# Kernel tuning notes

Hardware: AMD Instinct MI355X
Metric: run time of the kernel (lower is better)

Reference implementation:

```python
import jax, jax.numpy as jnp
import numpy as np

B, N, D, DEPTH = 1, 512, 128, 4


def mlp_apply(W, x):
    # W: (depth, d, d), x: (..., d). First layer has no activation, then silu before each matmul.
    x = x @ W[0]
    for i in range(1, DEPTH):
        x = jax.nn.silu(x) @ W[i]
    return x


def _binop(x, y):
    # linear recurrence combine: s_t = a_t * s_{t-1} + b_t
    a1, b1 = x
    a2, b2 = y
    return (a1 * a2, a2 * b1 + b2)


def setup_inputs() -> dict:
    key = jax.random.key(0)
    ks = jax.random.split(key, 7)
    s = 0.02  # scale for projection weights (torch Linear-like init magnitude)
    return {
        "seq": jax.random.normal(ks[0], (B, N, D), jnp.float32),
        "W_mem": jax.random.normal(ks[1], (DEPTH, D, D), jnp.float32) * (D ** -0.5),
        "W_q": jax.random.normal(ks[2], (D, D), jnp.float32) * s,
        "W_kv": jax.random.normal(ks[3], (D, 2 * D), jnp.float32) * s,
        "W_mom": jax.random.normal(ks[4], (D, 1), jnp.float32) * s,
        "W_step": jax.random.normal(ks[5], (D, 1), jnp.float32) * s,
        "W_decay": jax.random.normal(ks[6], (D, 1), jnp.float32) * s,
    }


def reference(seq, W_mem, W_q, W_kv, W_mom, W_step, W_decay):
    b, n, d = seq.shape
    # --- store_memories ---
    adaptive_lr = (seq @ W_step)[..., 0]            # (b, n)
    adaptive_mom = seq @ W_mom                      # (b, n, 1)
    decay = jax.nn.sigmoid(seq @ W_decay)           # (b, n, 1)

    kv = seq.reshape(b * n, d) @ W_kv               # (bn, 2d)
    keys, values = kv[:, :d], kv[:, d:]

    def loss_fn(W, k, v):
        pred = mlp_apply(W, k)                      # (d,)
        # (pred - v)^2 .mean(-1).sum() for a single sample == mean over d
        return jnp.mean((pred - v) ** 2)

    # per-sample meta-gradients wrt memory MLP weights
    losses, grads = jax.vmap(jax.value_and_grad(loss_fn, argnums=0), in_axes=(None, 0, 0))(W_mem, keys, values)
    grads = grads.reshape(b, n, DEPTH, d, d)
    surprise = grads * (-adaptive_lr)[..., None, None, None]   # (b,n,depth,d,d)

    # momentum_t = adaptive_mom_t * momentum_{t-1} + surprise_t  (assoc. scan over n)
    am = adaptive_mom[..., None, None]              # (b, n, 1, 1, 1)
    _, momentum = jax.lax.associative_scan(_binop, (am, surprise), axis=1)

    # update_t = (1 - decay_t) * update_{t-1} + momentum_t
    dec = (1.0 - decay)[..., None, None]            # (b, n, 1, 1, 1)
    _, updates = jax.lax.associative_scan(_binop, (dec, momentum), axis=1)

    # --- retrieve_memories with per-token updated weights ---
    q = (seq @ W_q).reshape(b * n, d)
    W_tok = (W_mem[None, None] + updates).reshape(b * n, DEPTH, d, d)
    retrieved = jax.vmap(mlp_apply)(W_tok, q).reshape(b, n, d)
    return retrieved
```

## Files before the change

kernel.cpp:

```cpp
#include <hip/hip_runtime.h>
#include <hip/hip_bf16.h>
#include <math.h>

#define N 512
#define NN (N*N)
#define D 128
#define DD (D*D)
#define ND (N*D)
#define LSTR 132
#define CSTR 68

__device__ __forceinline__ float sigmoidf_(float x) { return 1.f / (1.f + expf(-x)); }

__global__ void k_transpose(const float* __restrict__ W_mem, float* __restrict__ WT) {
    int idx = blockIdx.x * 256 + threadIdx.x;
    int l = idx / DD;
    int r = idx % DD;
    int i = r / D;
    int j = r % D;
    WT[idx] = W_mem[(l + 1) * DD + j * D + i];
}

__global__ __launch_bounds__(512) void k_phase1(
    const float* __restrict__ seq, const float* __restrict__ W_mem,
    const float* __restrict__ W_q, const float* __restrict__ W_kv,
    const float* __restrict__ W_mom, const float* __restrict__ W_step,
    const float* __restrict__ W_decay, const float* __restrict__ WT,
    float* __restrict__ Q, float* __restrict__ INS, float* __restrict__ ES,
    float* __restrict__ am, float* __restrict__ dec)
{
    __shared__ float s_seq[2][D];
    __shared__ float s_bufA[2][D];
    __shared__ float s_bufB[2][D];
    __shared__ float s_p3[4][2][3][D];
    __shared__ float s_part[4][2][D];
    __shared__ float s_red8[8][3];
    __shared__ float s_lr[2];

    const int tid = threadIdx.x;
    const int p   = tid >> 7;
    const int j   = tid & 127;
    const int t0  = blockIdx.x * 2;
    const int i0  = p * 32;

    if (p < 2) s_seq[p][j] = seq[(t0 + p) * D + j];
    __syncthreads();

    {
        const int wv   = tid >> 6;
        const int tok  = wv >> 2;
        const int half = (wv >> 1) & 1;
        float sv = s_seq[tok][j];
        float p0 = 0.f, p1 = 0.f, p2 = 0.f;
        if (half == 0) { p0 = sv * W_step[j]; p1 = sv * W_mom[j]; }
        else           { p2 = sv * W_decay[j]; }
#pragma unroll
        for (int off = 32; off > 0; off >>= 1) {
            p0 += __shfl_down(p0, off);
            p1 += __shfl_down(p1, off);
            p2 += __shfl_down(p2, off);
        }
        if ((tid & 63) == 0) {
            s_red8[wv][0] = p0; s_red8[wv][1] = p1; s_red8[wv][2] = p2;
        }
    }
    __syncthreads();
    if (tid < 2) {
        int b = tid * 4;
        s_lr[tid]  = s_red8[b][0] + s_red8[b + 1][0];
        am[t0+tid] = s_red8[b][1] + s_red8[b + 1][1];
        dec[t0+tid]= 1.f - sigmoidf_(s_red8[b + 2][2] + s_red8[b + 3][2]);
    }

    float k0 = 0.f, v0 = 0.f, q0 = 0.f;
    float k1 = 0.f, v1 = 0.f, q1 = 0.f;
#pragma unroll 8
    for (int ii = 0; ii < 32; ii++) {
        int i = i0 + ii;
        float wk = W_kv[i * 256 + j];
        float wq = W_q[i * 128 + j];
        float wvv = W_kv[i * 256 + 128 + j];
        float a0 = s_seq[0][i], a1 = s_seq[1][i];
        k0 += a0 * wk;  k1 += a1 * wk;
        v0 += a0 * wvv; v1 += a1 * wvv;
        q0 += a0 * wq;  q1 += a1 * wq;
    }
    s_p3[p][0][0][j] = k0; s_p3[p][0][1][j] = v0; s_p3[p][0][2][j] = q0;
    s_p3[p][1][0][j] = k1; s_p3[p][1][1][j] = v1; s_p3[p][1][2][j] = q1;
    __syncthreads();

    float vj = 0.f;
    if (p < 2) {
        const int tok = p;
        float kj = s_p3[0][tok][0][j] + s_p3[1][tok][0][j] + s_p3[2][tok][0][j] + s_p3[3][tok][0][j];
        vj       = s_p3[0][tok][1][j] + s_p3[1][tok][1][j] + s_p3[2][tok][1][j] + s_p3[3][tok][1][j];
        float qj = s_p3[0][tok][2][j] + s_p3[1][tok][2][j] + s_p3[2][tok][2][j] + s_p3[3][tok][2][j];
        Q[(t0 + tok) * D + j] = qj;
        INS[(t0 + tok) * D + j] = kj;
        s_bufA[tok][j] = kj;
    }
    __syncthreads();

    float hreg[4];
    float pred = 0.f;
    {
        float (*bufs[2])[D] = { s_bufA, s_bufB };
        for (int l = 0; l < 4; l++) {
            float (*cur)[D] = bufs[l & 1];
            float (*nxt)[D] = bufs[(l + 1) & 1];
            const float* Wp = W_mem + l * DD + j;
            float a0 = 0.f, a1 = 0.f;
#pragma unroll 8
            for (int ii = 0; ii < 32; ii++) {
                int i = i0 + ii;
                float w = Wp[i * D];
                a0 += cur[0][i] * w;
                a1 += cur[1][i] * w;
            }
            s_part[p][0][j] = a0;
            s_part[p][1][j] = a1;
            __syncthreads();
            if (p < 2) {
                const int tok = p;
                float y = (s_part[0][tok][j] + s_part[1][tok][j])
                        + (s_part[2][tok][j] + s_part[3][tok][j]);
                hreg[l] = y;
                if (l < 3) {
                    float a = y * sigmoidf_(y);
                    nxt[tok][j] = a;
                    INS[(l + 1) * ND + (t0 + tok) * D + j] = a;
                } else {
                    pred = y;
                }
            }
            __syncthreads();
        }

        if (p < 2) {
            const int tok = p;
            float e = -s_lr[tok] * (2.f / (float)D) * (pred - vj);
            ES[3 * ND + (t0 + tok) * D + j] = e;
            bufs[0][tok][j] = e;
        }
        __syncthreads();

        for (int l = 3; l >= 1; l--) {
            float (*cur)[D] = bufs[(3 - l) & 1];
            float (*nxt)[D] = bufs[(3 - l + 1) & 1];
            const float* Wp = WT + (l - 1) * DD + j;
            float a0 = 0.f, a1 = 0.f;
#pragma unroll 8
            for (int ii = 0; ii < 32; ii++) {
                int i = i0 + ii;
                float w = Wp[i * D];
                a0 += cur[0][i] * w;
                a1 += cur[1][i] * w;
            }
            s_part[p][0][j] = a0;
            s_part[p][1][j] = a1;
            __syncthreads();
            if (p < 2) {
                const int tok = p;
                float g = (s_part[0][tok][j] + s_part[1][tok][j])
                        + (s_part[2][tok][j] + s_part[3][tok][j]);
                float h = hreg[l - 1];
                float sg = sigmoidf_(h);
                float e2 = g * (sg * (1.f + h * (1.f - sg)));
                ES[(l - 1) * ND + (t0 + tok) * D + j] = e2;
                nxt[tok][j] = e2;
            }
            __syncthreads();
        }
    }
}

__global__ __launch_bounds__(512) void k_logscan(
    const float* __restrict__ am, const float* __restrict__ dec,
    double* __restrict__ LA, double* __restrict__ LDp, int* __restrict__ NC)
{
    __shared__ double sa[N], sd[N];
    __shared__ int sn[N];
    const int t = threadIdx.x;
    float a = am[t];
    float d = dec[t];
    sa[t] = log((double)fmaxf(fabsf(a), 1e-38f));
    sd[t] = log((double)fmaxf(d, 1e-38f));
    sn[t] = (a < 0.f) ? 1 : 0;
    __syncthreads();
    for (int off = 1; off < N; off <<= 1) {
        double va = 0.0, vd = 0.0; int vn = 0;
        if (t >= off) { va = sa[t - off]; vd = sd[t - off]; vn = sn[t - off]; }
        __syncthreads();
        sa[t] += va; sd[t] += vd; sn[t] += vn;
        __syncthreads();
    }
    LA[t] = sa[t]; LDp[t] = sd[t]; NC[t] = sn[t];
}

__global__ __launch_bounds__(256) void k_betamm(
    const double* __restrict__ LA, const double* __restrict__ LDp,
    const int* __restrict__ NC, float* __restrict__ betaP)
{
    const int bs = blockIdx.x;
    const int bt = blockIdx.y;
    const int z  = blockIdx.z;
    if (bs > bt) return;
    const int span = bt - bs + 1;
    const int chunk = (span + 3) >> 2;
    const int kBeg = bs + z * chunk;
    const int kEnd = (kBeg + chunk < bt + 1) ? (kBeg + chunk) : (bt + 1);
    if (kBeg >= kEnd) return;

    __shared__ float sA[32 * 34];
    __shared__ float sDT[32 * 34];

    const int tid = threadIdx.x;
    const int tx = tid & 15;
    const int ty = tid >> 4;
    float acc00 = 0.f, acc01 = 0.f, acc10 = 0.f, acc11 = 0.f;

    for (int kt = kBeg; kt < kEnd; kt++) {
        for (int i = tid; i < 1024; i += 256) {
            int r = i >> 5, c = i & 31;
            int u2 = kt * 32 + r, s2 = bs * 32 + c;
            float va = 0.f;
            if (s2 <= u2) {
                va = expf((float)(LA[u2] - LA[s2]));
                if ((NC[u2] - NC[s2]) & 1) va = -va;
            }
            sA[r * 34 + c] = va;
            int u1 = bt * 32 + r, s1 = kt * 32 + c;
            sDT[c * 34 + r] = (s1 <= u1) ? expf((float)(LDp[u1] - LDp[s1])) : 0.f;
        }
        __syncthreads();
#pragma unroll 8
        for (int k = 0; k < 32; k++) {
            float2 a = *(float2*)&sA[k * 34 + 2 * tx];
            float2 d = *(float2*)&sDT[k * 34 + 2 * ty];
            acc00 += d.x * a.x; acc01 += d.x * a.y;
            acc10 += d.y * a.x; acc11 += d.y * a.y;
        }
        __syncthreads();
    }
    float* bp = betaP + z * NN + (bt * 32 + 2 * ty) * N + bs * 32 + 2 * tx;
    *(float2*)bp       = make_float2(acc00, acc01);
    *(float2*)(bp + N) = make_float2(acc10, acc11);
}

__device__ __forceinline__ float beta_at(const float* __restrict__ betaP, int t, int s) {
    int bt = t >> 5, bs = s >> 5;
    if (bs > bt) return 0.f;
    int span = bt - bs + 1;
    int chunk = (span + 3) >> 2;
    int nz = (span + chunk - 1) / chunk;
    float v = betaP[t * N + s];
    for (int z = 1; z < nz; z++) v += betaP[z * NN + t * N + s];
    return v;
}

__global__ __launch_bounds__(256) void k_layer(
    const float* __restrict__ Xsrc, float* __restrict__ Pout,
    const float* __restrict__ Wl, const float* __restrict__ INSl,
    const float* __restrict__ ESl, const float* __restrict__ betaP,
    int mode)
{
    const int r = blockIdx.x;
    const int z = blockIdx.y;
    const bool isW = (z == 8);
    if (!isW && 4 * z > r) return;
    const int t0 = r * 16;
    const int lane = threadIdx.x;

    __shared__ __align__(16) float sX[16 * LSTR];
    __shared__ __align__(16) float sI[64 * LSTR];
    __shared__ __align__(16) float sE[32 * LSTR];
    __shared__ __align__(16) float sc[16 * CSTR];

    const int nzs = (r >> 2) + 1;
#pragma unroll
    for (int i = 0; i < 2; i++) {
        int f4 = lane + 256 * i;
        int row = f4 >> 5, c4 = f4 & 31;
        float4 v = ((const float4*)(Xsrc + t0 * D))[f4];
        if (mode) {
            for (int zz = 1; zz < nzs; zz++) {
                float4 u = ((const float4*)(Xsrc + zz * ND + t0 * D))[f4];
                v.x += u.x; v.y += u.y; v.z += u.z; v.w += u.w;
            }
            float4 w = ((const float4*)(Xsrc + 8 * ND + t0 * D))[f4];
            v.x += w.x; v.y += w.y; v.z += w.z; v.w += w.w;
            v.x = v.x * sigmoidf_(v.x); v.y = v.y * sigmoidf_(v.y);
            v.z = v.z * sigmoidf_(v.z); v.w = v.w * sigmoidf_(v.w);
        }
        *(float4*)(sX + row * LSTR + c4 * 4) = v;
    }

    if (isW) {
        __syncthreads();
        const int ti  = lane >> 4;
        const int j8  = (lane & 15) * 8;
        float acc[8];
#pragma unroll
        for (int b = 0; b < 8; b++) acc[b] = 0.f;
#pragma unroll 4
        for (int k = 0; k < D; k++) {
            float4 w0 = *(const float4*)(Wl + k * D + j8);
            float4 w1 = *(const float4*)(Wl + k * D + j8 + 4);
            float xv = sX[ti * LSTR + k];
            acc[0] += xv * w0.x; acc[1] += xv * w0.y;
            acc[2] += xv * w0.z; acc[3] += xv * w0.w;
            acc[4] += xv * w1.x; acc[5] += xv * w1.y;
            acc[6] += xv * w1.z; acc[7] += xv * w1.w;
        }
        float* yp = Pout + 8 * ND + (t0 + ti) * D + j8;
        *(float4*)yp       = make_float4(acc[0], acc[1], acc[2], acc[3]);
        *(float4*)(yp + 4) = make_float4(acc[4], acc[5], acc[6], acc[7]);
        return;
    }

    const int s0 = z * 64;
#pragma unroll
    for (int i = 0; i < 8; i++) {
        int f4 = lane + 256 * i;
        int row = f4 >> 5, c4 = f4 & 31;
        float4 a = ((const float4*)(INSl + s0 * D))[f4];
        *(float4*)(sI + row * LSTR + c4 * 4) = a;
    }

    const int rp = lane >> 5;
    const int sp = lane & 31;
    float b00 = beta_at(betaP, t0 + 2 * rp,     s0 + sp);
    float b01 = beta_at(betaP, t0 + 2 * rp,     s0 + sp + 32);
    float b10 = beta_at(betaP, t0 + 2 * rp + 1, s0 + sp);
    float b11 = beta_at(betaP, t0 + 2 * rp + 1, s0 + sp + 32);
    __syncthreads();

    float g00 = 0.f, g01 = 0.f, g10 = 0.f, g11 = 0.f;
#pragma unroll 8
    for (int k4 = 0; k4 < D; k4 += 4) {
        float4 a0 = *(float4*)(sX + (2 * rp) * LSTR + k4);
        float4 a1 = *(float4*)(sX + (2 * rp + 1) * LSTR + k4);
        float4 p0 = *(float4*)(sI + sp * LSTR + k4);
        float4 p1 = *(float4*)(sI + (sp + 32) * LSTR + k4);
        g00 += a0.x * p0.x + a0.y * p0.y + a0.z * p0.z + a0.w * p0.w;
        g01 += a0.x * p1.x + a0.y * p1.y + a0.z * p1.z + a0.w * p1.w;
        g10 += a1.x * p0.x + a1.y * p0.y + a1.z * p0.z + a1.w * p0.w;
        g11 += a1.x * p1.x + a1.y * p1.y + a1.z * p1.z + a1.w * p1.w;
    }
    sc[(2 * rp) * CSTR + sp]          = g00 * b00;
    sc[(2 * rp) * CSTR + sp + 32]     = g01 * b01;
    sc[(2 * rp + 1) * CSTR + sp]      = g10 * b10;
    sc[(2 * rp + 1) * CSTR + sp + 32] = g11 * b11;

    const int tp = lane >> 5;
    const int jc = (lane & 31) * 4;
    float acc[2][4];
#pragma unroll
    for (int a = 0; a < 2; a++)
#pragma unroll
        for (int b = 0; b < 4; b++) acc[a][b] = 0.f;

    for (int sub = 0; sub < 2; sub++) {
        __syncthreads();
#pragma unroll
        for (int i = 0; i < 4; i++) {
            int f4 = lane + 256 * i;
            int row = f4 >> 5, c4 = f4 & 31;
            float4 b = ((const float4*)(ESl + (s0 + sub * 32) * D))[f4];
            *(float4*)(sE + row * LSTR + c4 * 4) = b;
        }
        __syncthreads();
        const float* scp0 = sc + tp * CSTR + sub * 32;
        const float* scp1 = sc + (tp + 8) * CSTR + sub * 32;
#pragma unroll 8
        for (int s = 0; s < 32; s++) {
            float c0 = scp0[s];
            float c1 = scp1[s];
            float4 e = *(float4*)(sE + s * LSTR + jc);
            acc[0][0] += c0 * e.x; acc[0][1] += c0 * e.y;
            acc[0][2] += c0 * e.z; acc[0][3] += c0 * e.w;
            acc[1][0] += c1 * e.x; acc[1][1] += c1 * e.y;
            acc[1][2] += c1 * e.z; acc[1][3] += c1 * e.w;
        }
    }

    float* yp0 = Pout + z * ND + (t0 + tp) * D + jc;
    float* yp1 = Pout + z * ND + (t0 + tp + 8) * D + jc;
    *(float4*)yp0 = make_float4(acc[0][0], acc[0][1], acc[0][2], acc[0][3]);
    *(float4*)yp1 = make_float4(acc[1][0], acc[1][1], acc[1][2], acc[1][3]);
}

__global__ __launch_bounds__(256) void k_reduce(
    const float* __restrict__ P, float* __restrict__ out)
{
    int f4 = blockIdx.x * 256 + threadIdx.x;
    int t = f4 >> 5;
    int r = t >> 4;
    int nzs = (r >> 2) + 1;
    float4 v = ((const float4*)P)[f4];
    for (int zz = 1; zz < nzs; zz++) {
        float4 u = ((const float4*)(P + zz * ND))[f4];
        v.x += u.x; v.y += u.y; v.z += u.z; v.w += u.w;
    }
    float4 w = ((const float4*)(P + 8 * ND))[f4];
    v.x += w.x; v.y += w.y; v.z += w.z; v.w += w.w;
    ((float4*)out)[f4] = v;
}

extern "C" void kernel_launch(void* const* d_in, const int* in_sizes, int n_in,
                              void* d_out, int out_size, void* d_ws, size_t ws_size,
                              hipStream_t stream) {
    const float* seq     = (const float*)d_in[0];
    const float* W_mem   = (const float*)d_in[1];
    const float* W_q     = (const float*)d_in[2];
    const float* W_kv    = (const float*)d_in[3];
    const float* W_mom   = (const float*)d_in[4];
    const float* W_step  = (const float*)d_in[5];
    const float* W_decay = (const float*)d_in[6];
    float* out = (float*)d_out;

    float* ws    = (float*)d_ws;
    float* am    = ws;
    float* dec   = am + N;
    float* Q     = dec + N;
    float* INS   = Q + ND;
    float* ES    = INS + 4 * ND;
    float* betaP = ES + 4 * ND;
    float* Pa    = betaP + 4 * NN;
    float* Pb    = Pa + 9 * ND;
    float* WT    = Pb + 9 * ND;
    double* LA   = (double*)(WT + 3 * DD);
    double* LDp  = LA + N;
    int* NC      = (int*)(LDp + N);

    k_transpose<<<192, 256, 0, stream>>>(W_mem, WT);
    k_phase1<<<N / 2, 512, 0, stream>>>(seq, W_mem, W_q, W_kv, W_mom, W_step, W_decay,
                                        WT, Q, INS, ES, am, dec);
    k_logscan<<<1, N, 0, stream>>>(am, dec, LA, LDp, NC);
    dim3 mmgrid(N / 32, N / 32, 4);
    k_betamm<<<mmgrid, 256, 0, stream>>>(LA, LDp, NC, betaP);

    dim3 lgrid(32, 9);
    k_layer<<<lgrid, 256, 0, stream>>>(Q,  Pa, W_mem,          INS,          ES,          betaP, 0);
    k_layer<<<lgrid, 256, 0, stream>>>(Pa, Pb, W_mem + DD,     INS + ND,     ES + ND,     betaP, 1);
    k_layer<<<lgrid, 256, 0, stream>>>(Pb, Pa, W_mem + 2 * DD, INS + 2 * ND, ES + 2 * ND, betaP, 1);
    k_layer<<<lgrid, 256, 0, stream>>>(Pa, Pb, W_mem + 3 * DD, INS + 3 * ND, ES + 3 * ND, betaP, 1);
    k_reduce<<<64, 256, 0, stream>>>(Pb, out);
}
```

Measured before the change: 163.5 us.

## Fuse four layer kernels and reduce into one persistent kernel with per-row flags

Replaces the four k_layer launches and the k_reduce launch with a single kernel that loops over the layers. Blocks wait on per-row-tile atomic counters (acquire/release, agent scope) instead of kernel boundaries, and the W-column block performs the final reduction. Flags are zeroed in the transpose kernel. This removes four launch gaps and lets row tiles advance through layers independently, but it depends on all 288 blocks being co-resident, since the spin-waits could deadlock otherwise, and it keeps four separate P buffers.

```diff
diff --git a/kernel.cpp b/kernel.cpp
--- a/kernel.cpp
+++ b/kernel.cpp
@@ -9,11 +9,14 @@
 #define ND (N*D)
 #define LSTR 132
 #define CSTR 68
+#define PSZ (9*ND)
 
 __device__ __forceinline__ float sigmoidf_(float x) { return 1.f / (1.f + expf(-x)); }
 
-__global__ void k_transpose(const float* __restrict__ W_mem, float* __restrict__ WT) {
+__global__ void k_transpose(const float* __restrict__ W_mem, float* __restrict__ WT,
+                            int* __restrict__ flags) {
     int idx = blockIdx.x * 256 + threadIdx.x;
+    if (blockIdx.x == 0 && threadIdx.x < 128) flags[threadIdx.x] = 0;
     int l = idx / DD;
     int r = idx % DD;
     int i = r / D;
@@ -258,11 +261,11 @@
     return v;
 }
 
-__global__ __launch_bounds__(256) void k_layer(
-    const float* __restrict__ Xsrc, float* __restrict__ Pout,
-    const float* __restrict__ Wl, const float* __restrict__ INSl,
-    const float* __restrict__ ESl, const float* __restrict__ betaP,
-    int mode)
+__global__ __launch_bounds__(256) void k_mega(
+    const float* __restrict__ Q, float* __restrict__ out,
+    const float* __restrict__ W_mem, const float* __restrict__ INS,
+    const float* __restrict__ ES, const float* __restrict__ betaP,
+    float* __restrict__ P, int* __restrict__ flags)
 {
     const int r = blockIdx.x;
     const int z = blockIdx.y;
@@ -270,141 +273,168 @@
     if (!isW && 4 * z > r) return;
     const int t0 = r * 16;
     const int lane = threadIdx.x;
+    const int nzs = (r >> 2) + 1;
+    const int target = nzs + 1;
 
     __shared__ __align__(16) float sX[16 * LSTR];
     __shared__ __align__(16) float sI[64 * LSTR];
     __shared__ __align__(16) float sE[32 * LSTR];
     __shared__ __align__(16) float sc[16 * CSTR];
 
-    const int nzs = (r >> 2) + 1;
-#pragma unroll
-    for (int i = 0; i < 2; i++) {
-        int f4 = lane + 256 * i;
-        int row = f4 >> 5, c4 = f4 & 31;
-        float4 v = ((const float4*)(Xsrc + t0 * D))[f4];
-        if (mode) {
-            for (int zz = 1; zz < nzs; zz++) {
-                float4 u = ((const float4*)(Xsrc + zz * ND + t0 * D))[f4];
-                v.x += u.x; v.y += u.y; v.z += u.z; v.w += u.w;
-            }
-            float4 w = ((const float4*)(Xsrc + 8 * ND + t0 * D))[f4];
-            v.x += w.x; v.y += w.y; v.z += w.z; v.w += w.w;
-            v.x = v.x * sigmoidf_(v.x); v.y = v.y * sigmoidf_(v.y);
-            v.z = v.z * sigmoidf_(v.z); v.w = v.w * sigmoidf_(v.w);
-        }
-        *(float4*)(sX + row * LSTR + c4 * 4) = v;
-    }
-
-    if (isW) {
-        __syncthreads();
-        const int ti  = lane >> 4;
-        const int j8  = (lane & 15) * 8;
-        float acc[8];
-#pragma unroll
-        for (int b = 0; b < 8; b++) acc[b] = 0.f;
-#pragma unroll 4
-        for (int k = 0; k < D; k++) {
-            float4 w0 = *(const float4*)(Wl + k * D + j8);
-            float4 w1 = *(const float4*)(Wl + k * D + j8 + 4);
-            float xv = sX[ti * LSTR + k];
-            acc[0] += xv * w0.x; acc[1] += xv * w0.y;
-            acc[2] += xv * w0.z; acc[3] += xv * w0.w;
-            acc[4] += xv * w1.x; acc[5] += xv * w1.y;
-            acc[6] += xv * w1.z; acc[7] += xv * w1.w;
-        }
-        float* yp = Pout + 8 * ND + (t0 + ti) * D + j8;
-        *(float4*)yp       = make_float4(acc[0], acc[1], acc[2], acc[3]);
-        *(float4*)(yp + 4) = make_float4(acc[4], acc[5], acc[6], acc[7]);
-        return;
-    }
-
-    const int s0 = z * 64;
-#pragma unroll
-    for (int i = 0; i < 8; i++) {
-        int f4 = lane + 256 * i;
-        int row = f4 >> 5, c4 = f4 & 31;
-        float4 a = ((const float4*)(INSl + s0 * D))[f4];
-        *(float4*)(sI + row * LSTR + c4 * 4) = a;
-    }
-
-    const int rp = lane >> 5;
-    const int sp = lane & 31;
-    float b00 = beta_at(betaP, t0 + 2 * rp,     s0 + sp);
-    float b01 = beta_at(betaP, t0 + 2 * rp,     s0 + sp + 32);
-    float b10 = beta_at(betaP, t0 + 2 * rp + 1, s0 + sp);
-    float b11 = beta_at(betaP, t0 + 2 * rp + 1, s0 + sp + 32);
-    __syncthreads();
-
-    float g00 = 0.f, g01 = 0.f, g10 = 0.f, g11 = 0.f;
-#pragma unroll 8
-    for (int k4 = 0; k4 < D; k4 += 4) {
-        float4 a0 = *(float4*)(sX + (2 * rp) * LSTR + k4);
-        float4 a1 = *(float4*)(sX + (2 * rp + 1) * LSTR + k4);
-        float4 p0 = *(float4*)(sI + sp * LSTR + k4);
-        float4 p1 = *(float4*)(sI + (sp + 32) * LSTR + k4);
-        g00 += a0.x * p0.x + a0.y * p0.y + a0.z * p0.z + a0.w * p0.w;
-        g01 += a0.x * p1.x + a0.y * p1.y + a0.z * p1.z + a0.w * p1.w;
-        g10 += a1.x * p0.x + a1.y * p0.y + a1.z * p0.z + a1.w * p0.w;
-        g11 += a1.x * p1.x + a1.y * p1.y + a1.z * p1.z + a1.w * p1.w;
-    }
-    sc[(2 * rp) * CSTR + sp]          = g00 * b00;
-    sc[(2 * rp) * CSTR + sp + 32]     = g01 * b01;
-    sc[(2 * rp + 1) * CSTR + sp]      = g10 * b10;
-    sc[(2 * rp + 1) * CSTR + sp + 32] = g11 * b11;
-
-    const int tp = lane >> 5;
-    const int jc = (lane & 31) * 4;
-    float acc[2][4];
-#pragma unroll
-    for (int a = 0; a < 2; a++)
-#pragma unroll
-        for (int b = 0; b < 4; b++) acc[a][b] = 0.f;
-
-    for (int sub = 0; sub < 2; sub++) {
-        __syncthreads();
-#pragma unroll
-        for (int i = 0; i < 4; i++) {
+    for (int l = 0; l < 4; l++) {
+        const float* Wl   = W_mem + l * DD;
+        const float* INSl = INS + l * ND;
+        const float* ESl  = ES + l * ND;
+        const float* Xsrc = (l == 0) ? Q : (P + (l - 1) * PSZ);
+        float* Pout = P + l * PSZ;
+
+        if (l > 0) {
+            if (lane == 0) {
+                while (__hip_atomic_load(&flags[(l - 1) * 32 + r], __ATOMIC_ACQUIRE,
+                                         __HIP_MEMORY_SCOPE_AGENT) < target)
+                    __builtin_amdgcn_s_sleep(2);
+            }
+            __syncthreads();
+        }
+
+#pragma unroll
+        for (int i = 0; i < 2; i++) {
             int f4 = lane + 256 * i;
             int row = f4 >> 5, c4 = f4 & 31;
-            float4 b = ((const float4*)(ESl + (s0 + sub * 32) * D))[f4];
-            *(float4*)(sE + row * LSTR + c4 * 4) = b;
-        }
-        __syncthreads();
-        const float* scp0 = sc + tp * CSTR + sub * 32;
-        const float* scp1 = sc + (tp + 8) * CSTR + sub * 32;
-#pragma unroll 8
-        for (int s = 0; s < 32; s++) {
-            float c0 = scp0[s];
-            float c1 = scp1[s];
-            float4 e = *(float4*)(sE + s * LSTR + jc);
-            acc[0][0] += c0 * e.x; acc[0][1] += c0 * e.y;
-            acc[0][2] += c0 * e.z; acc[0][3] += c0 * e.w;
-            acc[1][0] += c1 * e.x; acc[1][1] += c1 * e.y;
-            acc[1][2] += c1 * e.z; acc[1][3] += c1 * e.w;
-        }
-    }
-
-    float* yp0 = Pout + z * ND + (t0 + tp) * D + jc;
-    float* yp1 = Pout + z * ND + (t0 + tp + 8) * D + jc;
-    *(float4*)yp0 = make_float4(acc[0][0], acc[0][1], acc[0][2], acc[0][3]);
-    *(float4*)yp1 = make_float4(acc[1][0], acc[1][1], acc[1][2], acc[1][3]);
-}
-
-__global__ __launch_bounds__(256) void k_reduce(
-    const float* __restrict__ P, float* __restrict__ out)
-{
-    int f4 = blockIdx.x * 256 + threadIdx.x;
-    int t = f4 >> 5;
-    int r = t >> 4;
-    int nzs = (r >> 2) + 1;
-    float4 v = ((const float4*)P)[f4];
-    for (int zz = 1; zz < nzs; zz++) {
-        float4 u = ((const float4*)(P + zz * ND))[f4];
-        v.x += u.x; v.y += u.y; v.z += u.z; v.w += u.w;
-    }
-    float4 w = ((const float4*)(P + 8 * ND))[f4];
-    v.x += w.x; v.y += w.y; v.z += w.z; v.w += w.w;
-    ((float4*)out)[f4] = v;
+            float4 v = ((const float4*)(Xsrc + t0 * D))[f4];
+            if (l > 0) {
+                for (int zz = 1; zz < nzs; zz++) {
+                    float4 u = ((const float4*)(Xsrc + zz * ND + t0 * D))[f4];
+                    v.x += u.x; v.y += u.y; v.z += u.z; v.w += u.w;
+                }
+                float4 w = ((const float4*)(Xsrc + 8 * ND + t0 * D))[f4];
+                v.x += w.x; v.y += w.y; v.z += w.z; v.w += w.w;
+                v.x = v.x * sigmoidf_(v.x); v.y = v.y * sigmoidf_(v.y);
+                v.z = v.z * sigmoidf_(v.z); v.w = v.w * sigmoidf_(v.w);
+            }
+            *(float4*)(sX + row * LSTR + c4 * 4) = v;
+        }
+
+        if (isW) {
+            __syncthreads();
+            const int ti  = lane >> 4;
+            const int j8  = (lane & 15) * 8;
+            float acc[8];
+#pragma unroll
+            for (int b = 0; b < 8; b++) acc[b] = 0.f;
+#pragma unroll 4
+            for (int k = 0; k < D; k++) {
+                float4 w0 = *(const float4*)(Wl + k * D + j8);
+                float4 w1 = *(const float4*)(Wl + k * D + j8 + 4);
+                float xv = sX[ti * LSTR + k];
+                acc[0] += xv * w0.x; acc[1] += xv * w0.y;
+                acc[2] += xv * w0.z; acc[3] += xv * w0.w;
+                acc[4] += xv * w1.x; acc[5] += xv * w1.y;
+                acc[6] += xv * w1.z; acc[7] += xv * w1.w;
+            }
+            float* yp = Pout + 8 * ND + (t0 + ti) * D + j8;
+            *(float4*)yp       = make_float4(acc[0], acc[1], acc[2], acc[3]);
+            *(float4*)(yp + 4) = make_float4(acc[4], acc[5], acc[6], acc[7]);
+        } else {
+            const int s0 = z * 64;
+#pragma unroll
+            for (int i = 0; i < 8; i++) {
+                int f4 = lane + 256 * i;
+                int row = f4 >> 5, c4 = f4 & 31;
+                float4 a = ((const float4*)(INSl + s0 * D))[f4];
+                *(float4*)(sI + row * LSTR + c4 * 4) = a;
+            }
+
+            const int rp = lane >> 5;
+            const int sp = lane & 31;
+            float b00 = beta_at(betaP, t0 + 2 * rp,     s0 + sp);
+            float b01 = beta_at(betaP, t0 + 2 * rp,     s0 + sp + 32);
+            float b10 = beta_at(betaP, t0 + 2 * rp + 1, s0 + sp);
+            float b11 = beta_at(betaP, t0 + 2 * rp + 1, s0 + sp + 32);
+            __syncthreads();
+
+            float g00 = 0.f, g01 = 0.f, g10 = 0.f, g11 = 0.f;
+#pragma unroll 8
+            for (int k4 = 0; k4 < D; k4 += 4) {
+                float4 a0 = *(float4*)(sX + (2 * rp) * LSTR + k4);
+                float4 a1 = *(float4*)(sX + (2 * rp + 1) * LSTR + k4);
+                float4 p0 = *(float4*)(sI + sp * LSTR + k4);
+                float4 p1 = *(float4*)(sI + (sp + 32) * LSTR + k4);
+                g00 += a0.x * p0.x + a0.y * p0.y + a0.z * p0.z + a0.w * p0.w;
+                g01 += a0.x * p1.x + a0.y * p1.y + a0.z * p1.z + a0.w * p1.w;
+                g10 += a1.x * p0.x + a1.y * p0.y + a1.z * p0.z + a1.w * p0.w;
+                g11 += a1.x * p1.x + a1.y * p1.y + a1.z * p1.z + a1.w * p1.w;
+            }
+            sc[(2 * rp) * CSTR + sp]          = g00 * b00;
+            sc[(2 * rp) * CSTR + sp + 32]     = g01 * b01;
+            sc[(2 * rp + 1) * CSTR + sp]      = g10 * b10;
+            sc[(2 * rp + 1) * CSTR + sp + 32] = g11 * b11;
+
+            const int tp = lane >> 5;
+            const int jc = (lane & 31) * 4;
+            float acc[2][4];
+#pragma unroll
+            for (int a = 0; a < 2; a++)
+#pragma unroll
+                for (int b = 0; b < 4; b++) acc[a][b] = 0.f;
+
+            for (int sub = 0; sub < 2; sub++) {
+                __syncthreads();
+#pragma unroll
+                for (int i = 0; i < 4; i++) {
+                    int f4 = lane + 256 * i;
+                    int row = f4 >> 5, c4 = f4 & 31;
+                    float4 b = ((const float4*)(ESl + (s0 + sub * 32) * D))[f4];
+                    *(float4*)(sE + row * LSTR + c4 * 4) = b;
+                }
+                __syncthreads();
+                const float* scp0 = sc + tp * CSTR + sub * 32;
+                const float* scp1 = sc + (tp + 8) * CSTR + sub * 32;
+#pragma unroll 8
+                for (int s = 0; s < 32; s++) {
+                    float c0 = scp0[s];
+                    float c1 = scp1[s];
+                    float4 e = *(float4*)(sE + s * LSTR + jc);
+                    acc[0][0] += c0 * e.x; acc[0][1] += c0 * e.y;
+                    acc[0][2] += c0 * e.z; acc[0][3] += c0 * e.w;
+                    acc[1][0] += c1 * e.x; acc[1][1] += c1 * e.y;
+                    acc[1][2] += c1 * e.z; acc[1][3] += c1 * e.w;
+                }
+            }
+
+            float* yp0 = Pout + z * ND + (t0 + tp) * D + jc;
+            float* yp1 = Pout + z * ND + (t0 + tp + 8) * D + jc;
+            *(float4*)yp0 = make_float4(acc[0][0], acc[0][1], acc[0][2], acc[0][3]);
+            *(float4*)yp1 = make_float4(acc[1][0], acc[1][1], acc[1][2], acc[1][3]);
+        }
+
+        __syncthreads();
+        if (lane == 0)
+            __hip_atomic_fetch_add(&flags[l * 32 + r], 1, __ATOMIC_RELEASE,
+                                   __HIP_MEMORY_SCOPE_AGENT);
+    }
+
+    if (isW) {
+        if (lane == 0) {
+            while (__hip_atomic_load(&flags[3 * 32 + r], __ATOMIC_ACQUIRE,
+                                     __HIP_MEMORY_SCOPE_AGENT) < target)
+                __builtin_amdgcn_s_sleep(2);
+        }
+        __syncthreads();
+        const float* Pf = P + 3 * PSZ;
+#pragma unroll
+        for (int i = 0; i < 2; i++) {
+            int f4 = lane + 256 * i;
+            float4 v = ((const float4*)(Pf + t0 * D))[f4];
+            for (int zz = 1; zz < nzs; zz++) {
+                float4 u = ((const float4*)(Pf + zz * ND + t0 * D))[f4];
+                v.x += u.x; v.y += u.y; v.z += u.z; v.w += u.w;
+            }
+            float4 w = ((const float4*)(Pf + 8 * ND + t0 * D))[f4];
+            v.x += w.x; v.y += w.y; v.z += w.z; v.w += w.w;
+            ((float4*)(out + t0 * D))[f4] = v;
+        }
+    }
 }
 
 extern "C" void kernel_launch(void* const* d_in, const int* in_sizes, int n_in,
@@ -426,24 +456,20 @@
     float* INS   = Q + ND;
     float* ES    = INS + 4 * ND;
     float* betaP = ES + 4 * ND;
-    float* Pa    = betaP + 4 * NN;
-    float* Pb    = Pa + 9 * ND;
-    float* WT    = Pb + 9 * ND;
+    float* P     = betaP + 4 * NN;
+    float* WT    = P + 4 * PSZ;
     double* LA   = (double*)(WT + 3 * DD);
     double* LDp  = LA + N;
     int* NC      = (int*)(LDp + N);
-
-    k_transpose<<<192, 256, 0, stream>>>(W_mem, WT);
+    int* flags   = NC + N;
+
+    k_transpose<<<192, 256, 0, stream>>>(W_mem, WT, flags);
     k_phase1<<<N / 2, 512, 0, stream>>>(seq, W_mem, W_q, W_kv, W_mom, W_step, W_decay,
                                         WT, Q, INS, ES, am, dec);
     k_logscan<<<1, N, 0, stream>>>(am, dec, LA, LDp, NC);
     dim3 mmgrid(N / 32, N / 32, 4);
     k_betamm<<<mmgrid, 256, 0, stream>>>(LA, LDp, NC, betaP);
 
-    dim3 lgrid(32, 9);
-    k_layer<<<lgrid, 256, 0, stream>>>(Q,  Pa, W_mem,          INS,          ES,          betaP, 0);
-    k_layer<<<lgrid, 256, 0, stream>>>(Pa, Pb, W_mem + DD,     INS + ND,     ES + ND,     betaP, 1);
-    k_layer<<<lgrid, 256, 0, stream>>>(Pb, Pa, W_mem + 2 * DD, INS + 2 * ND, ES + 2 * ND, betaP, 1);
-    k_layer<<<lgrid, 256, 0, stream>>>(Pa, Pb, W_mem + 3 * DD, INS + 3 * ND, ES + 3 * ND, betaP, 1);
-    k_reduce<<<64, 256, 0, stream>>>(Pb, out);
-}
+    dim3 mgrid(32, 9);
+    k_mega<<<mgrid, 256, 0, stream>>>(Q, out, W_mem, INS, ES, betaP, P, flags);
+}
```

Result: slower. 235.9 us (+44.2%).
